# Optimization experiments

Hardware: AMD Instinct MI355X
Metric: run time of the kernel (lower is better)

## Reference

```python
import math
import jax, jax.numpy as jnp
import numpy as np

IMAGE_SIZE = (256, 704)
N_VOX = (200, 200, 4)
VOX_SIZE = (0.5, 0.5, 1.5)
BN_EPS = 1e-5


def _voxel_points_homog():
    # matches get_points: meshgrid(indexing='ij') * voxel_size + origin, origin = [0,0,-1] - n_vox/2*vox
    nx, ny, nz = N_VOX
    idx = jnp.stack(jnp.meshgrid(jnp.arange(nx), jnp.arange(ny), jnp.arange(nz), indexing='ij')).astype(jnp.float32)  # [3,nx,ny,nz]
    vs = jnp.array(VOX_SIZE, jnp.float32)
    origin = jnp.array([0.0, 0.0, -1.0], jnp.float32) - jnp.array(N_VOX, jnp.float32) / 2.0 * vs
    pts = idx * vs.reshape(3, 1, 1, 1) + origin.reshape(3, 1, 1, 1)
    P = nx * ny * nz
    pts = pts.reshape(3, P)
    return jnp.concatenate([pts, jnp.ones((1, P), jnp.float32)], axis=0)  # [4,P]


def _backproject(feat, proj, aug_t, stride):
    # feat: [N,C,H,W]; proj: [N,3,4]; aug_t: [N,2] (u,v translation from img_aug_matrix[:, :2, -1])
    N, C, H, W = feat.shape
    homog = _voxel_points_homog()            # [4,P]
    P = homog.shape[1]
    p2i = jnp.einsum('nij,jp->nip', proj, homog)  # [N,3,P]
    Z = p2i[:, 2]
    Zs = jnp.where(jnp.abs(Z) > 1e-6, Z, 1e-6)    # guard div-by-0; such points are invalid anyway
    u = p2i[:, 0] / Zs + aug_t[:, 0:1]
    v = p2i[:, 1] / Zs + aug_t[:, 1:2]
    u_fm = jnp.round(u / stride).astype(jnp.int32)
    v_fm = jnp.round(v / stride).astype(jnp.int32)
    valid = (u_fm >= 0) & (v_fm >= 0) & (u_fm < W) & (v_fm < H) & (Z > 0)  # [N,P]
    sel = (N - 1) - jnp.argmax(valid[::-1], axis=0)   # [P]
    any_valid = valid.any(axis=0)                     # [P]
    ar = jnp.arange(P)
    u_s = jnp.clip(u_fm[sel, ar], 0, W - 1)
    v_s = jnp.clip(v_fm[sel, ar], 0, H - 1)
    g = feat[sel, :, v_s, u_s]                        # [P,C] single fused gather
    vol = (g * any_valid[:, None].astype(feat.dtype)).T  # [C,P]
    return vol.reshape(C, *N_VOX)


def _forward(mlvl_feats, points, lidar2image, img_aug_matrix, lidar_aug_matrix,
             conv_w, conv_b, bn_gamma, bn_beta, bn_mean, bn_var):
    stride = float(math.ceil(IMAGE_SIZE[1] / mlvl_feats.shape[-1]))  # static

    def per_batch(feat, iam, lam, l2i):
        iam_r = iam.at[..., -1].set(0.0)                 # zero last column
        proj = (iam_r @ l2i @ lam[None])[:, :3, :]       # [N,3,4]
        aug_t = iam[:, 0:2, -1]                          # [N,2]
        return _backproject(feat, proj, aug_t, stride)

    vols = jax.vmap(per_batch)(mlvl_feats, img_aug_matrix, lidar_aug_matrix, lidar2image)  # [B,C,nx,ny,nz]
    w = jnp.transpose(points, (0, 2, 3, 1))[:, None]     # [B,1,nx,ny,nz]
    bev = (vols * w).sum(axis=-1)                        # [B,C,nx,ny]  (cat of single z-slice)
    y = jnp.einsum('bchw,oc->bohw', bev, conv_w) + conv_b[None, :, None, None]
    inv = jax.lax.rsqrt(bn_var + BN_EPS)
    y = (y - bn_mean[None, :, None, None]) * (inv * bn_gamma)[None, :, None, None] + bn_beta[None, :, None, None]
    return jax.nn.relu(y)


def setup_inputs() -> dict:
    key = jax.random.key(0)
    ks = jax.random.split(key, 12)
    B, N, C, H, W = 1, 6, 256, 32, 88
    return {
        'mlvl_feats': jax.random.normal(ks[0], (B, N, C, H, W), jnp.float32),
        'points': jax.random.uniform(ks[1], (B, N_VOX[2], N_VOX[0], N_VOX[1]), jnp.float32),
        'ori_points': 0,
        'img': 0,
        'lidar2camera': jax.random.normal(ks[2], (B, N, 4, 4), jnp.float32),
        'lidar2image': jax.random.normal(ks[3], (B, N, 4, 4), jnp.float32),
        'cam_intrinsic': jax.random.normal(ks[4], (B, N, 4, 4), jnp.float32),
        'cam_2_lidar': jax.random.normal(ks[5], (B, N, 4, 4), jnp.float32),
        'img_aug_matrix': jnp.eye(4, dtype=jnp.float32)[None, None] + 0.1 * jax.random.normal(ks[6], (B, N, 4, 4), jnp.float32),
        'lidar_aug_matrix': jnp.eye(4, dtype=jnp.float32)[None] + 0.1 * jax.random.normal(ks[7], (B, 4, 4), jnp.float32),
        'img_metas': 0,
        'conv_w': 0.02 * jax.random.normal(ks[8], (80, 256), jnp.float32),
        'conv_b': jax.random.normal(ks[9], (80,), jnp.float32) * 0.01,
        'bn_gamma': jnp.ones((80,), jnp.float32),
        'bn_beta': jnp.zeros((80,), jnp.float32),
        'bn_mean': jnp.zeros((80,), jnp.float32),
        'bn_var': jnp.ones((80,), jnp.float32),
    }


def reference(mlvl_feats, points, ori_points, img, lidar2camera, lidar2image,
              cam_intrinsic, cam_2_lidar, img_aug_matrix, lidar_aug_matrix,
              img_metas, conv_w, conv_b, bn_gamma, bn_beta, bn_mean, bn_var):
    return _forward(mlvl_feats, points, lidar2image, img_aug_matrix, lidar_aug_matrix,
                    conv_w, conv_b, bn_gamma, bn_beta, bn_mean, bn_var)
```

## Files before the change

### kernel.cpp

```cpp
#include <hip/hip_runtime.h>
#include <math.h>

typedef __attribute__((ext_vector_type(8))) short bf16x8;
typedef __attribute__((ext_vector_type(4))) float f32x4;

#define N_CAM 6
#define C_IN 256
#define C_OUT 80
#define FH 32
#define FW 88
#define NXG 200
#define NYG 200
#define S_SPATIAL (NXG*NYG)
#define POS_PER_CAM (FH*FW)
#define NPOS (N_CAM*POS_PER_CAM)
#define TPOS 32

#define WS_WF     0
#define WS_FEAT2B 10240

__device__ __forceinline__ unsigned short f2bf(float f) {
    unsigned u = __builtin_bit_cast(unsigned, f);
    u += 0x7fffu + ((u >> 16) & 1u);
    return (unsigned short)(u >> 16);
}
__device__ __forceinline__ float bf2f(unsigned short u) {
    return __builtin_bit_cast(float, ((unsigned)u) << 16);
}

__global__ __launch_bounds__(64) void k_prep(const float* __restrict__ conv_w,
                                             const float* __restrict__ gamma,
                                             const float* __restrict__ var,
                                             uint4* __restrict__ wf) {
    int fi = blockIdx.x;
    int t = threadIdx.x;
    int nt = fi >> 3, ks = fi & 7;
    int o  = nt * 16 + (t & 15);
    int cb = ks * 32 + (t >> 4) * 8;
    float inv = 1.0f / sqrtf(var[o] + 1e-5f);
    float sc = __fmul_rn(inv, gamma[o]);
    const float* wrow = conv_w + o * C_IN + cb;
    unsigned short e[8];
    #pragma unroll
    for (int j = 0; j < 8; ++j)
        e[j] = f2bf(__fmul_rn(wrow[j], sc));
    uint4 u;
    u.x = e[0] | ((unsigned)e[1] << 16);
    u.y = e[2] | ((unsigned)e[3] << 16);
    u.z = e[4] | ((unsigned)e[5] << 16);
    u.w = e[6] | ((unsigned)e[7] << 16);
    wf[fi * 64 + t] = u;
}

__global__ __launch_bounds__(128) void k_fconv(const float* __restrict__ feat,
                                               const bf16x8* __restrict__ wf,
                                               unsigned short* __restrict__ feat2b) {
    __shared__ uint4 sfo[1024];
    int b = blockIdx.x, t = threadIdx.x;
    int n = b / 88, p0 = (b % 88) * TPOS;
    const float* fn = feat + (size_t)n * C_IN * POS_PER_CAM + p0;
    uint2* sfo2 = reinterpret_cast<uint2*>(sfo);

    #pragma unroll
    for (int i = 0; i < 16; ++i) {
        int task = i * 128 + t;
        int pl = task & 31, cg = task >> 5;
        int c0 = cg * 4;
        float v0 = fn[(c0+0) * POS_PER_CAM + pl];
        float v1 = fn[(c0+1) * POS_PER_CAM + pl];
        float v2 = fn[(c0+2) * POS_PER_CAM + pl];
        float v3 = fn[(c0+3) * POS_PER_CAM + pl];
        unsigned lo = f2bf(v0) | ((unsigned)f2bf(v1) << 16);
        unsigned hi = f2bf(v2) | ((unsigned)f2bf(v3) << 16);
        int ksp = c0 >> 5;
        int q   = (c0 & 31) >> 3;
        int lf  = (pl & 15) + (q << 4);
        int f   = ((pl >> 4) * 8 + ksp) * 64 + lf;
        sfo2[f * 2 + (cg & 1)] = make_uint2(lo, hi);
    }
    __syncthreads();

    int wv = t >> 6, l = t & 63;
    const bf16x8* sfrag = reinterpret_cast<const bf16x8*>(sfo);
    bf16x8 a[8];
    #pragma unroll
    for (int ks = 0; ks < 8; ++ks)
        a[ks] = sfrag[(wv * 8 + ks) * 64 + l];
    int posb = b * TPOS + wv * 16 + ((l >> 4) << 2);
    #pragma unroll
    for (int nt = 0; nt < 5; ++nt) {
        f32x4 acc = {0.f, 0.f, 0.f, 0.f};
        #pragma unroll
        for (int ks = 0; ks < 8; ++ks) {
            bf16x8 bb = wf[(nt * 8 + ks) * 64 + l];
            acc = __builtin_amdgcn_mfma_f32_16x16x32_bf16(a[ks], bb, acc, 0, 0, 0);
        }
        #pragma unroll
        for (int r = 0; r < 4; ++r)
            feat2b[(size_t)(posb + r) * C_OUT + nt * 16 + (l & 15)] = f2bf(acc[r]);
    }
}

__global__ __launch_bounds__(256) void k_main(const unsigned short* __restrict__ feat2b,
                                              const float* __restrict__ iam,
                                              const float* __restrict__ lam,
                                              const float* __restrict__ l2i,
                                              const float* __restrict__ conv_b,
                                              const float* __restrict__ gamma,
                                              const float* __restrict__ beta,
                                              const float* __restrict__ mean,
                                              const float* __restrict__ var,
                                              const float* __restrict__ points,
                                              float* __restrict__ out) {
    __shared__ float s_pa[84];
    __shared__ float s_bias[C_OUT];
    __shared__ int   s_base[256];
    __shared__ float s_w[256];
    __shared__ float s_y[64 * 81];
    int t = threadIdx.x;
    int col0 = blockIdx.x * 64;

    if (t < N_CAM) {
        int n = t;
        const float* A = iam + n * 16;
        const float* L = l2i + n * 16;
        float M1[12];
        #pragma unroll
        for (int i = 0; i < 3; ++i)
            #pragma unroll
            for (int j = 0; j < 4; ++j) {
                float acc = __fmul_rn(A[i*4+0], L[0*4+j]);
                acc = __fmaf_rn(A[i*4+1], L[1*4+j], acc);
                acc = __fmaf_rn(A[i*4+2], L[2*4+j], acc);
                M1[i*4+j] = acc;
            }
        #pragma unroll
        for (int i = 0; i < 3; ++i)
            #pragma unroll
            for (int j = 0; j < 4; ++j) {
                float acc = __fmul_rn(M1[i*4+0], lam[0*4+j]);
                acc = __fmaf_rn(M1[i*4+1], lam[1*4+j], acc);
                acc = __fmaf_rn(M1[i*4+2], lam[2*4+j], acc);
                acc = __fmaf_rn(M1[i*4+3], lam[3*4+j], acc);
                s_pa[n*12 + i*4 + j] = acc;
            }
        s_pa[72 + n*2 + 0] = A[0*4 + 3];
        s_pa[72 + n*2 + 1] = A[1*4 + 3];
    } else if (t >= 64 && t < 64 + C_OUT) {
        int o = t - 64;
        float inv = 1.0f / sqrtf(var[o] + 1e-5f);
        float sc = __fmul_rn(inv, gamma[o]);
        s_bias[o] = __fadd_rn(__fmul_rn(__fsub_rn(conv_b[o], mean[o]), sc), beta[o]);
    }
    __syncthreads();

    {
        int cl = t & 63, z = t >> 6;
        int col = col0 + cl;
        int ix = col / NYG, iy = col % NYG;
        float x  = (float)ix * 0.5f - 50.0f;
        float y  = (float)iy * 0.5f - 50.0f;
        float zc = (float)z  * 1.5f - 4.0f;
        int sel_base = 0;
        bool any = false;
        #pragma unroll
        for (int n = 0; n < N_CAM; ++n) {
            const float* P = s_pa + n * 12;
            float px = __fadd_rn(__fadd_rn(__fadd_rn(__fmul_rn(P[0], x), __fmul_rn(P[1], y)), __fmul_rn(P[2], zc)), P[3]);
            float py = __fadd_rn(__fadd_rn(__fadd_rn(__fmul_rn(P[4], x), __fmul_rn(P[5], y)), __fmul_rn(P[6], zc)), P[7]);
            float pz = __fadd_rn(__fadd_rn(__fadd_rn(__fmul_rn(P[8], x), __fmul_rn(P[9], y)), __fmul_rn(P[10], zc)), P[11]);
            float Z = pz;
            float Zs = (fabsf(Z) > 1e-6f) ? Z : 1e-6f;
            float u = __fadd_rn(px / Zs, s_pa[72 + n*2 + 0]);
            float v = __fadd_rn(py / Zs, s_pa[72 + n*2 + 1]);
            float uf = rintf(__fmul_rn(u, 0.125f));
            float vf = rintf(__fmul_rn(v, 0.125f));
            int ui = (int)uf, vi = (int)vf;
            bool val = (ui >= 0) & (vi >= 0) & (ui < FW) & (vi < FH) & (Z > 0.0f);
            if (val) { sel_base = ((n * FH + vi) * FW + ui) * C_OUT; any = true; }
        }
        float w = 0.0f;
        if (any) w = points[z * S_SPATIAL + col];
        else sel_base = 0;
        s_base[z * 64 + cl] = sel_base;
        s_w[z * 64 + cl] = w;
    }
    __syncthreads();

    #pragma unroll
    for (int it = 0; it < 3; ++it) {
        int task = it * 256 + t;
        if (task < 640) {
            int c = task / 10, o8 = task - c * 10;
            uint4 v0 = reinterpret_cast<const uint4*>(feat2b + s_base[0*64 + c])[o8];
            uint4 v1 = reinterpret_cast<const uint4*>(feat2b + s_base[1*64 + c])[o8];
            uint4 v2 = reinterpret_cast<const uint4*>(feat2b + s_base[2*64 + c])[o8];
            uint4 v3 = reinterpret_cast<const uint4*>(feat2b + s_base[3*64 + c])[o8];
            float w0 = s_w[0*64 + c], w1 = s_w[1*64 + c];
            float w2 = s_w[2*64 + c], w3 = s_w[3*64 + c];
            #pragma unroll
            for (int e = 0; e < 8; ++e) {
                unsigned u0 = (&v0.x)[e >> 1], u1 = (&v1.x)[e >> 1];
                unsigned u2 = (&v2.x)[e >> 1], u3 = (&v3.x)[e >> 1];
                int sh = (e & 1) << 4;
                float f0 = bf2f((unsigned short)(u0 >> sh));
                float f1 = bf2f((unsigned short)(u1 >> sh));
                float f2 = bf2f((unsigned short)(u2 >> sh));
                float f3 = bf2f((unsigned short)(u3 >> sh));
                float acc =            __fmul_rn(w0, f0);
                acc = __fadd_rn(acc, __fmul_rn(w1, f1));
                acc = __fadd_rn(acc, __fmul_rn(w2, f2));
                acc = __fadd_rn(acc, __fmul_rn(w3, f3));
                int o = o8 * 8 + e;
                float yv = fmaxf(__fadd_rn(acc, s_bias[o]), 0.0f);
                s_y[c * 81 + o] = yv;
            }
        }
    }
    __syncthreads();

    #pragma unroll
    for (int it = 0; it < 20; ++it) {
        int idx = it * 256 + t;
        int o = idx >> 6, c = idx & 63;
        out[o * S_SPATIAL + col0 + c] = s_y[c * 81 + o];
    }
}

extern "C" void kernel_launch(void* const* d_in, const int* in_sizes, int n_in,
                              void* d_out, int out_size, void* d_ws, size_t ws_size,
                              hipStream_t stream) {
    const float* feat   = (const float*)d_in[0];
    const float* points = (const float*)d_in[1];
    const float* l2i    = (const float*)d_in[5];
    const float* iam    = (const float*)d_in[8];
    const float* lam    = (const float*)d_in[9];
    const float* conv_w = (const float*)d_in[11];
    const float* conv_b = (const float*)d_in[12];
    const float* gamma  = (const float*)d_in[13];
    const float* beta   = (const float*)d_in[14];
    const float* mean   = (const float*)d_in[15];
    const float* var    = (const float*)d_in[16];

    float* ws = (float*)d_ws;
    uint4* wf = (uint4*)(ws + WS_WF);
    unsigned short* feat2b = (unsigned short*)(ws + WS_FEAT2B);
    float* out = (float*)d_out;

    hipLaunchKernelGGL(k_prep, dim3(40), dim3(64), 0, stream,
                       conv_w, gamma, var, wf);
    hipLaunchKernelGGL(k_fconv, dim3(NPOS / TPOS), dim3(128), 0, stream,
                       feat, (const bf16x8*)wf, feat2b);
    hipLaunchKernelGGL(k_main, dim3(S_SPATIAL / 64), dim3(256), 0, stream,
                       feat2b, iam, lam, l2i, conv_b, gamma, beta, mean, var,
                       points, out);
}
```

Measured before the change: 22.70 us.

## Repartition feature conv: one 16-position tile per block, one output tile per wave

The 1x1 conv kernel now handles 16 positions per block with 5 waves, each wave computing one 16-channel output tile, instead of 32 positions per block with 2 waves each looping over all 5 output tiles. This doubles the block count (1056 blocks) and spreads the MFMA work over more waves, aiming at better GPU occupancy and latency hiding on a small kernel. In exchange, each A-fragment is loaded by five waves instead of one, and the weight fragments are re-read by more blocks. The other edits only rename local variables.

```diff
diff --git a/kernel.cpp b/kernel.cpp
--- a/kernel.cpp
+++ b/kernel.cpp
@@ -14,7 +14,8 @@
 #define S_SPATIAL (NXG*NYG)
 #define POS_PER_CAM (FH*FW)
 #define NPOS (N_CAM*POS_PER_CAM)
-#define TPOS 32
+#define MT_PER_CAM (POS_PER_CAM/16)
+#define NMT (NPOS/16)
 
 #define WS_WF     0
 #define WS_FEAT2B 10240
@@ -52,53 +53,52 @@
     wf[fi * 64 + t] = u;
 }
 
-__global__ __launch_bounds__(128) void k_fconv(const float* __restrict__ feat,
+__global__ __launch_bounds__(320) void k_fconv(const float* __restrict__ feat,
                                                const bf16x8* __restrict__ wf,
                                                unsigned short* __restrict__ feat2b) {
-    __shared__ uint4 sfo[1024];
+    __shared__ uint4 sfo[512];
     int b = blockIdx.x, t = threadIdx.x;
-    int n = b / 88, p0 = (b % 88) * TPOS;
+    int n = b / MT_PER_CAM, p0 = (b % MT_PER_CAM) * 16;
     const float* fn = feat + (size_t)n * C_IN * POS_PER_CAM + p0;
     uint2* sfo2 = reinterpret_cast<uint2*>(sfo);
 
     #pragma unroll
-    for (int i = 0; i < 16; ++i) {
-        int task = i * 128 + t;
-        int pl = task & 31, cg = task >> 5;
-        int c0 = cg * 4;
-        float v0 = fn[(c0+0) * POS_PER_CAM + pl];
-        float v1 = fn[(c0+1) * POS_PER_CAM + pl];
-        float v2 = fn[(c0+2) * POS_PER_CAM + pl];
-        float v3 = fn[(c0+3) * POS_PER_CAM + pl];
-        unsigned lo = f2bf(v0) | ((unsigned)f2bf(v1) << 16);
-        unsigned hi = f2bf(v2) | ((unsigned)f2bf(v3) << 16);
-        int ksp = c0 >> 5;
-        int q   = (c0 & 31) >> 3;
-        int lf  = (pl & 15) + (q << 4);
-        int f   = ((pl >> 4) * 8 + ksp) * 64 + lf;
-        sfo2[f * 2 + (cg & 1)] = make_uint2(lo, hi);
-    }
-    __syncthreads();
-
-    int wv = t >> 6, l = t & 63;
+    for (int i = 0; i < 4; ++i) {
+        int task = i * 320 + t;
+        if (task < 1024) {
+            int pl = task & 15, cg = task >> 4;
+            int c0 = cg * 4;
+            float v0 = fn[(c0+0) * POS_PER_CAM + pl];
+            float v1 = fn[(c0+1) * POS_PER_CAM + pl];
+            float v2 = fn[(c0+2) * POS_PER_CAM + pl];
+            float v3 = fn[(c0+3) * POS_PER_CAM + pl];
+            unsigned lo = f2bf(v0) | ((unsigned)f2bf(v1) << 16);
+            unsigned hi = f2bf(v2) | ((unsigned)f2bf(v3) << 16);
+            int ksp = c0 >> 5;
+            int q   = (c0 & 31) >> 3;
+            int lf  = pl + (q << 4);
+            int f   = ksp * 64 + lf;
+            sfo2[f * 2 + (cg & 1)] = make_uint2(lo, hi);
+        }
+    }
+    __syncthreads();
+
+    int nt = t >> 6, l = t & 63;
     const bf16x8* sfrag = reinterpret_cast<const bf16x8*>(sfo);
     bf16x8 a[8];
     #pragma unroll
     for (int ks = 0; ks < 8; ++ks)
-        a[ks] = sfrag[(wv * 8 + ks) * 64 + l];
-    int posb = b * TPOS + wv * 16 + ((l >> 4) << 2);
-    #pragma unroll
-    for (int nt = 0; nt < 5; ++nt) {
-        f32x4 acc = {0.f, 0.f, 0.f, 0.f};
-        #pragma unroll
-        for (int ks = 0; ks < 8; ++ks) {
-            bf16x8 bb = wf[(nt * 8 + ks) * 64 + l];
-            acc = __builtin_amdgcn_mfma_f32_16x16x32_bf16(a[ks], bb, acc, 0, 0, 0);
-        }
-        #pragma unroll
-        for (int r = 0; r < 4; ++r)
-            feat2b[(size_t)(posb + r) * C_OUT + nt * 16 + (l & 15)] = f2bf(acc[r]);
-    }
+        a[ks] = sfrag[ks * 64 + l];
+    int posb = b * 16 + ((l >> 4) << 2);
+    f32x4 acc = {0.f, 0.f, 0.f, 0.f};
+    #pragma unroll
+    for (int ks = 0; ks < 8; ++ks) {
+        bf16x8 bb = wf[(nt * 8 + ks) * 64 + l];
+        acc = __builtin_amdgcn_mfma_f32_16x16x32_bf16(a[ks], bb, acc, 0, 0, 0);
+    }
+    #pragma unroll
+    for (int r = 0; r < 4; ++r)
+        feat2b[(size_t)(posb + r) * C_OUT + nt * 16 + (l & 15)] = f2bf(acc[r]);
 }
 
 __global__ __launch_bounds__(256) void k_main(const unsigned short* __restrict__ feat2b,
@@ -171,10 +171,10 @@
             float pz = __fadd_rn(__fadd_rn(__fadd_rn(__fmul_rn(P[8], x), __fmul_rn(P[9], y)), __fmul_rn(P[10], zc)), P[11]);
             float Z = pz;
             float Zs = (fabsf(Z) > 1e-6f) ? Z : 1e-6f;
-            float u = __fadd_rn(px / Zs, s_pa[72 + n*2 + 0]);
-            float v = __fadd_rn(py / Zs, s_pa[72 + n*2 + 1]);
-            float uf = rintf(__fmul_rn(u, 0.125f));
-            float vf = rintf(__fmul_rn(v, 0.125f));
+            float uu = __fadd_rn(px / Zs, s_pa[72 + n*2 + 0]);
+            float vv = __fadd_rn(py / Zs, s_pa[72 + n*2 + 1]);
+            float uf = rintf(__fmul_rn(uu, 0.125f));
+            float vf = rintf(__fmul_rn(vv, 0.125f));
             int ui = (int)uf, vi = (int)vf;
             bool val = (ui >= 0) & (vi >= 0) & (ui < FW) & (vi < FH) & (Z > 0.0f);
             if (val) { sel_base = ((n * FH + vi) * FW + ui) * C_OUT; any = true; }
@@ -245,13 +245,13 @@
     float* ws = (float*)d_ws;
     uint4* wf = (uint4*)(ws + WS_WF);
     unsigned short* feat2b = (unsigned short*)(ws + WS_FEAT2B);
-    float* out = (float*)d_out;
+    float* outp = (float*)d_out;
 
     hipLaunchKernelGGL(k_prep, dim3(40), dim3(64), 0, stream,
                        conv_w, gamma, var, wf);
-    hipLaunchKernelGGL(k_fconv, dim3(NPOS / TPOS), dim3(128), 0, stream,
+    hipLaunchKernelGGL(k_fconv, dim3(NMT), dim3(320), 0, stream,
                        feat, (const bf16x8*)wf, feat2b);
     hipLaunchKernelGGL(k_main, dim3(S_SPATIAL / 64), dim3(256), 0, stream,
                        feat2b, iam, lam, l2i, conv_b, gamma, beta, mean, var,
-                       points, out);
-}
+                       points, outp);
+}
```

Result: slower. 26.06 us (+14.8%).
